# Kernel optimization log

Measured on AMD Instinct MI355X. Metric: run time of the kernel, lower is better.

Reference implementation:

```python
import jax, jax.numpy as jnp
import numpy as np

MASK_SUB = 1000000.0  # the module subtracts 1e6 from masked scores (not -inf)

def setup_inputs() -> dict:
    key = jax.random.key(0)
    kq, kk, kv = jax.random.split(key, 3)
    B, S, D = 16, 2048, 64
    q = jax.random.normal(kq, (B, S, D), dtype=jnp.float32)
    k = jax.random.normal(kk, (B, S, D), dtype=jnp.float32)
    v = jax.random.normal(kv, (B, S, D), dtype=jnp.float32)
    return {"q": q, "k": k, "v": v}

def reference(q, k, v):
    d_k = k.shape[-1]
    s = k.shape[-2]
    # scores: [b, s_q, s_k]
    scores = jnp.einsum('bqd,bkd->bqk', q, k) / jnp.sqrt(jnp.asarray(d_k, q.dtype))
    # causal mask: strictly-upper-triangular entries get 1e6 subtracted (matches torch.triu diagonal=1)
    causal = jnp.triu(jnp.ones((s, s), dtype=bool), k=1)
    scores = jnp.where(causal[None, :, :], scores - MASK_SUB, scores)
    weights = jax.nn.softmax(scores, axis=-1)
    return jnp.einsum('bqk,bkd->bqd', weights, v)
```

## Files before the change

kernel.cpp:

```cpp
#include <hip/hip_runtime.h>
#include <stdint.h>


typedef __bf16 bf16x8 __attribute__((ext_vector_type(8)));
typedef float f32x4 __attribute__((ext_vector_type(4)));

#define NB 16
#define SL 2048
#define DH 64

__device__ __forceinline__ __bf16 f2bf(float f) {
    uint32_t u = __builtin_bit_cast(uint32_t, f);
    u += 0x7FFFu + ((u >> 16) & 1u);
    uint16_t h = (uint16_t)(u >> 16);
    return __builtin_bit_cast(__bf16, h);
}

__device__ __forceinline__ void load_lds16(const void* g, void* l) {
    __builtin_amdgcn_global_load_lds(
        (const __attribute__((address_space(1))) uint32_t*)g,
        (__attribute__((address_space(3))) uint32_t*)l, 16, 0, 0);
}

__global__ __launch_bounds__(256) void prepass(
        const float* __restrict__ K, const float* __restrict__ V,
        __bf16* __restrict__ Kb, __bf16* __restrict__ Vt) {
    __shared__ float tl[64][68];
    const int b    = blockIdx.x >> 5;
    const int tile = blockIdx.x & 31;
    const int s0   = tile << 6;
    const int t    = threadIdx.x;
    const int r    = t >> 2;
    const int c0   = (t & 3) * 16;

    const float* Kp = K + ((size_t)(b * SL + s0) + r) * DH + c0;
    float4 f0 = ((const float4*)Kp)[0], f1 = ((const float4*)Kp)[1];
    float4 f2 = ((const float4*)Kp)[2], f3 = ((const float4*)Kp)[3];
    bf16x8 w0, w1;
    w0[0]=f2bf(f0.x); w0[1]=f2bf(f0.y); w0[2]=f2bf(f0.z); w0[3]=f2bf(f0.w);
    w0[4]=f2bf(f1.x); w0[5]=f2bf(f1.y); w0[6]=f2bf(f1.z); w0[7]=f2bf(f1.w);
    w1[0]=f2bf(f2.x); w1[1]=f2bf(f2.y); w1[2]=f2bf(f2.z); w1[3]=f2bf(f2.w);
    w1[4]=f2bf(f3.x); w1[5]=f2bf(f3.y); w1[6]=f2bf(f3.z); w1[7]=f2bf(f3.w);
    __bf16* Kbp = Kb + ((size_t)(b * SL + s0) + r) * DH;
    const int j0 = c0 >> 3;
    *(bf16x8*)(Kbp + ((j0       ^ (r & 7)) * 8)) = w0;
    *(bf16x8*)(Kbp + (((j0 + 1) ^ (r & 7)) * 8)) = w1;

    const float* Vp = V + ((size_t)(b * SL + s0) + r) * DH + c0;
    ((float4*)&tl[r][c0])[0] = ((const float4*)Vp)[0];
    ((float4*)&tl[r][c0])[1] = ((const float4*)Vp)[1];
    ((float4*)&tl[r][c0])[2] = ((const float4*)Vp)[2];
    ((float4*)&tl[r][c0])[3] = ((const float4*)Vp)[3];
    __syncthreads();

    __bf16* img = Vt + ((size_t)(b * 32 + tile)) * 4096;
#pragma unroll
    for (int half = 0; half < 2; ++half) {
        const int c = half * 256 + t;
        const int d = c >> 3, slot = c & 7;
        const int jj = slot ^ (d & 7);
        bf16x8 w;
#pragma unroll
        for (int e = 0; e < 8; ++e) w[e] = f2bf(tl[jj * 8 + e][d]);
        *(bf16x8*)(img + c * 8) = w;
    }
}

__global__ __launch_bounds__(256, 2) void attn_fwd(
        const float* __restrict__ Q, const __bf16* __restrict__ Kb,
        const __bf16* __restrict__ Vt, float* __restrict__ part,
        float* __restrict__ lpart) {
    __shared__ __align__(16) __bf16 lK[3][4096];
    __shared__ __align__(16) __bf16 lV[3][4096];
    __shared__ __align__(16) __bf16 lP[4][2048];

    const int bid = blockIdx.x;
    const int b   = bid & 15;
    const int j   = 39 - (bid >> 4);
    int qb, c;
    if (j < 4)        { qb = j;                 c = 0; }
    else if (j < 12)  { qb = 4 + ((j - 4) >> 1);  c = (j - 4) & 1; }
    else if (j < 24)  { int k = j - 12; qb = 8 + k / 3;    c = k % 3; }
    else              { int k = j - 24; qb = 12 + (k >> 2); c = k & 3; }
    const int nt  = 2 * qb + 2;
    const int kt0 = c * 8;
    const int kt1 = min(kt0 + 8, nt);

    const int tid  = threadIdx.x;
    const int wave = tid >> 6, lane = tid & 63, quad = lane >> 4, l16 = lane & 15;
    const int xk   = l16 & 7;
    const int qg0  = qb * 128 + wave * 16 + l16;
    const int qg1  = qg0 + 64;

    const float QSC = 0.125f * 1.44269504088896340736f;
    bf16x8 qf[2][2];
#pragma unroll
    for (int st = 0; st < 2; ++st) {
        const float* qp = Q + ((size_t)b * SL + (st ? qg1 : qg0)) * DH;
#pragma unroll
        for (int s = 0; s < 2; ++s) {
            float4 a0 = ((const float4*)(qp + s * 32 + quad * 8))[0];
            float4 a1 = ((const float4*)(qp + s * 32 + quad * 8))[1];
            qf[st][s][0] = f2bf(a0.x * QSC); qf[st][s][1] = f2bf(a0.y * QSC);
            qf[st][s][2] = f2bf(a0.z * QSC); qf[st][s][3] = f2bf(a0.w * QSC);
            qf[st][s][4] = f2bf(a1.x * QSC); qf[st][s][5] = f2bf(a1.y * QSC);
            qf[st][s][6] = f2bf(a1.z * QSC); qf[st][s][7] = f2bf(a1.w * QSC);
        }
    }

    f32x4 acc0[4], acc1[4];
#pragma unroll
    for (int t = 0; t < 4; ++t) { acc0[t] = (f32x4)0.0f; acc1[t] = (f32x4)0.0f; }
    float ls0 = 0.0f, ls1 = 0.0f;

    const __bf16* Kbase = Kb + (size_t)b * SL * DH;
    const __bf16* Vbase = Vt + (size_t)b * 32 * 4096;
    __bf16* lPw = lP[wave];

    auto stage = [&](int kt2) {
        const int bufi = kt2 % 3;
        const __bf16* Ks = Kbase + (size_t)kt2 * 4096;
        const __bf16* Vs = Vbase + (size_t)kt2 * 4096;
#pragma unroll
        for (int i2 = 0; i2 < 2; ++i2) {
            load_lds16(Ks + (size_t)(i2 * 256 + tid) * 8,
                       &lK[bufi][(i2 * 256 + wave * 64) * 8]);
            load_lds16(Vs + (size_t)(i2 * 256 + tid) * 8,
                       &lV[bufi][(i2 * 256 + wave * 64) * 8]);
        }
    };

    auto softmax_store = [&](f32x4* sc, int soff, float& ls) {
#pragma unroll
        for (int t = 0; t < 4; ++t) {
            float p0 = __builtin_amdgcn_exp2f(sc[t][0]);
            float p1 = __builtin_amdgcn_exp2f(sc[t][1]);
            float p2 = __builtin_amdgcn_exp2f(sc[t][2]);
            float p3 = __builtin_amdgcn_exp2f(sc[t][3]);
            ls += (p0 + p1) + (p2 + p3);
            uint32_t u0 = __builtin_amdgcn_perm(__builtin_bit_cast(uint32_t, p1),
                                               __builtin_bit_cast(uint32_t, p0), 0x07060302u);
            uint32_t u1 = __builtin_amdgcn_perm(__builtin_bit_cast(uint32_t, p3),
                                               __builtin_bit_cast(uint32_t, p2), 0x07060302u);
            const int cw = 2 * t + (quad >> 1);
            uint2 val; val.x = u0; val.y = u1;
            *(uint2*)&lPw[soff + l16 * 64 + ((cw ^ xk) << 3) + ((quad & 1) << 2)] = val;
        }
    };

    __builtin_amdgcn_sched_barrier(0);
    stage(kt0);
    __builtin_amdgcn_sched_barrier(0);
    stage(kt0 + 1);

    for (int kt = kt0; kt < kt1; ++kt) {
        if (kt + 1 < kt1) asm volatile("s_waitcnt vmcnt(4)" ::: "memory");
        else              asm volatile("s_waitcnt vmcnt(0)" ::: "memory");
        __builtin_amdgcn_s_barrier();
        __builtin_amdgcn_sched_barrier(0);
        if (kt + 2 < kt1) stage(kt + 2);

        const __bf16* K_ = lK[kt % 3];
        const __bf16* V_ = lV[kt % 3];

        f32x4 sc0[4], sc1[4];
#pragma unroll
        for (int t = 0; t < 4; ++t) { sc0[t] = (f32x4)0.0f; sc1[t] = (f32x4)0.0f; }
        __builtin_amdgcn_s_setprio(1);
#pragma unroll
        for (int s = 0; s < 2; ++s) {
#pragma unroll
            for (int t = 0; t < 4; ++t) {
                bf16x8 kf = *(const bf16x8*)&K_[(t * 16 + l16) * 64 + (((s * 4 + quad) ^ xk) << 3)];
                sc0[t] = __builtin_amdgcn_mfma_f32_16x16x32_bf16(kf, qf[0][s], sc0[t], 0, 0, 0);
                sc1[t] = __builtin_amdgcn_mfma_f32_16x16x32_bf16(kf, qf[1][s], sc1[t], 0, 0, 0);
            }
        }
        __builtin_amdgcn_s_setprio(0);

        if (kt >= 2 * qb) {
            const int kb = kt * 64;
#pragma unroll
            for (int t = 0; t < 4; ++t)
#pragma unroll
                for (int r = 0; r < 4; ++r) {
                    const int key = kb + t * 16 + quad * 4 + r;
                    if (key > qg0) sc0[t][r] = -1.0e30f;
                    if (key > qg1) sc1[t][r] = -1.0e30f;
                }
        }

        const bool s0live = (kt != nt - 1);
        if (s0live) softmax_store(sc0, 0, ls0);
        softmax_store(sc1, 1024, ls1);
        asm volatile("" ::: "memory");

        bf16x8 pf10 = *(const bf16x8*)&lPw[1024 + l16 * 64 + (((0 + quad) ^ xk) << 3)];
        bf16x8 pf11 = *(const bf16x8*)&lPw[1024 + l16 * 64 + (((4 + quad) ^ xk) << 3)];

        __builtin_amdgcn_s_setprio(1);
        if (s0live) {
            bf16x8 pf00 = *(const bf16x8*)&lPw[l16 * 64 + (((0 + quad) ^ xk) << 3)];
            bf16x8 pf01 = *(const bf16x8*)&lPw[l16 * 64 + (((4 + quad) ^ xk) << 3)];
#pragma unroll
            for (int t = 0; t < 4; ++t) {
                bf16x8 vf = *(const bf16x8*)&V_[(t * 16 + l16) * 64 + (((0 + quad) ^ xk) << 3)];
                acc0[t] = __builtin_amdgcn_mfma_f32_16x16x32_bf16(vf, pf00, acc0[t], 0, 0, 0);
                acc1[t] = __builtin_amdgcn_mfma_f32_16x16x32_bf16(vf, pf10, acc1[t], 0, 0, 0);
            }
#pragma unroll
            for (int t = 0; t < 4; ++t) {
                bf16x8 vf = *(const bf16x8*)&V_[(t * 16 + l16) * 64 + (((4 + quad) ^ xk) << 3)];
                acc0[t] = __builtin_amdgcn_mfma_f32_16x16x32_bf16(vf, pf01, acc0[t], 0, 0, 0);
                acc1[t] = __builtin_amdgcn_mfma_f32_16x16x32_bf16(vf, pf11, acc1[t], 0, 0, 0);
            }
        } else {
#pragma unroll
            for (int t = 0; t < 4; ++t) {
                bf16x8 vf = *(const bf16x8*)&V_[(t * 16 + l16) * 64 + (((0 + quad) ^ xk) << 3)];
                acc1[t] = __builtin_amdgcn_mfma_f32_16x16x32_bf16(vf, pf10, acc1[t], 0, 0, 0);
            }
#pragma unroll
            for (int t = 0; t < 4; ++t) {
                bf16x8 vf = *(const bf16x8*)&V_[(t * 16 + l16) * 64 + (((4 + quad) ^ xk) << 3)];
                acc1[t] = __builtin_amdgcn_mfma_f32_16x16x32_bf16(vf, pf11, acc1[t], 0, 0, 0);
            }
        }
        __builtin_amdgcn_s_setprio(0);
    }

    ls0 += __shfl_xor(ls0, 16); ls0 += __shfl_xor(ls0, 32);
    ls1 += __shfl_xor(ls1, 16); ls1 += __shfl_xor(ls1, 32);

    float* pp0 = part + ((size_t)(b * SL + qg0) * 4 + c) * DH + quad * 4;
    float* pp1 = part + ((size_t)(b * SL + qg1) * 4 + c) * DH + quad * 4;
#pragma unroll
    for (int t = 0; t < 4; ++t) {
        float4 o4;
        o4.x = acc0[t][0]; o4.y = acc0[t][1]; o4.z = acc0[t][2]; o4.w = acc0[t][3];
        *(float4*)(pp0 + t * 16) = o4;
        o4.x = acc1[t][0]; o4.y = acc1[t][1]; o4.z = acc1[t][2]; o4.w = acc1[t][3];
        *(float4*)(pp1 + t * 16) = o4;
    }
    if (quad == 0) {
        lpart[(size_t)(b * SL + qg0) * 4 + c] = ls0;
        lpart[(size_t)(b * SL + qg1) * 4 + c] = ls1;
    }
}

__global__ __launch_bounds__(256) void combine(
        const float* __restrict__ part, const float* __restrict__ lpart,
        float* __restrict__ O) {
    const int tid = threadIdx.x;
    const int r   = blockIdx.x * 16 + (tid >> 4);
    const int d4  = tid & 15;
    const int qb  = (r >> 7) & 15;
    const int nch = (2 * qb + 9) >> 3;
    float4 s = make_float4(0.f, 0.f, 0.f, 0.f);
    float ls = 0.f;
    for (int c = 0; c < nch; ++c) {
        float4 p = *(const float4*)(part + ((size_t)r * 4 + c) * DH + d4 * 4);
        s.x += p.x; s.y += p.y; s.z += p.z; s.w += p.w;
        ls += lpart[(size_t)r * 4 + c];
    }
    const float inv = 1.0f / ls;
    float4 o; o.x = s.x * inv; o.y = s.y * inv; o.z = s.z * inv; o.w = s.w * inv;
    *(float4*)(O + (size_t)r * DH + d4 * 4) = o;
}

extern "C" void kernel_launch(void* const* d_in, const int* in_sizes, int n_in,
                              void* d_out, int out_size, void* d_ws, size_t ws_size,
                              hipStream_t stream) {
    const float* q = (const float*)d_in[0];
    const float* k = (const float*)d_in[1];
    const float* v = (const float*)d_in[2];
    float* o = (float*)d_out;
    __bf16* Kb   = (__bf16*)d_ws;
    __bf16* Vt   = Kb + (size_t)NB * SL * DH;
    float*  pt   = (float*)((char*)d_ws + (8u << 20));
    float*  lp   = pt + (size_t)NB * SL * 4 * DH;
    hipLaunchKernelGGL(prepass, dim3(NB * 32), dim3(256), 0, stream, k, v, Kb, Vt);
    hipLaunchKernelGGL(attn_fwd, dim3(640), dim3(256), 0, stream, q, Kb, Vt, pt, lp);
    hipLaunchKernelGGL(combine, dim3(NB * SL / 16), dim3(256), 0, stream, pt, lp, o);
}
```

Baseline: 106.2 us.

## Read K and V tiles directly from global memory instead of LDS staging

Removes the triple-buffered LDS staging of K and V tiles (global_load_lds plus waitcnt/barrier pipeline). Each wave now reads its K and V fragments straight from global memory through the cache. Occupancy is raised to 3 blocks per SM now that LDS use is smaller. This drops the barriers and LDS traffic, but exposes global-load latency and duplicate loads across waves, with no explicit prefetch.

```diff
diff --git a/kernel.cpp b/kernel.cpp
--- a/kernel.cpp
+++ b/kernel.cpp
@@ -14,12 +14,6 @@
     u += 0x7FFFu + ((u >> 16) & 1u);
     uint16_t h = (uint16_t)(u >> 16);
     return __builtin_bit_cast(__bf16, h);
-}
-
-__device__ __forceinline__ void load_lds16(const void* g, void* l) {
-    __builtin_amdgcn_global_load_lds(
-        (const __attribute__((address_space(1))) uint32_t*)g,
-        (__attribute__((address_space(3))) uint32_t*)l, 16, 0, 0);
 }
 
 __global__ __launch_bounds__(256) void prepass(
@@ -66,12 +60,10 @@
     }
 }
 
-__global__ __launch_bounds__(256, 2) void attn_fwd(
+__global__ __launch_bounds__(256, 3) void attn_fwd(
         const float* __restrict__ Q, const __bf16* __restrict__ Kb,
         const __bf16* __restrict__ Vt, float* __restrict__ part,
         float* __restrict__ lpart) {
-    __shared__ __align__(16) __bf16 lK[3][4096];
-    __shared__ __align__(16) __bf16 lV[3][4096];
     __shared__ __align__(16) __bf16 lP[4][2048];
 
     const int bid = blockIdx.x;
@@ -116,19 +108,6 @@
     const __bf16* Kbase = Kb + (size_t)b * SL * DH;
     const __bf16* Vbase = Vt + (size_t)b * 32 * 4096;
     __bf16* lPw = lP[wave];
-
-    auto stage = [&](int kt2) {
-        const int bufi = kt2 % 3;
-        const __bf16* Ks = Kbase + (size_t)kt2 * 4096;
-        const __bf16* Vs = Vbase + (size_t)kt2 * 4096;
-#pragma unroll
-        for (int i2 = 0; i2 < 2; ++i2) {
-            load_lds16(Ks + (size_t)(i2 * 256 + tid) * 8,
-                       &lK[bufi][(i2 * 256 + wave * 64) * 8]);
-            load_lds16(Vs + (size_t)(i2 * 256 + tid) * 8,
-                       &lV[bufi][(i2 * 256 + wave * 64) * 8]);
-        }
-    };
 
     auto softmax_store = [&](f32x4* sc, int soff, float& ls) {
 #pragma unroll
@@ -148,20 +127,9 @@
         }
     };
 
-    __builtin_amdgcn_sched_barrier(0);
-    stage(kt0);
-    __builtin_amdgcn_sched_barrier(0);
-    stage(kt0 + 1);
-
     for (int kt = kt0; kt < kt1; ++kt) {
-        if (kt + 1 < kt1) asm volatile("s_waitcnt vmcnt(4)" ::: "memory");
-        else              asm volatile("s_waitcnt vmcnt(0)" ::: "memory");
-        __builtin_amdgcn_s_barrier();
-        __builtin_amdgcn_sched_barrier(0);
-        if (kt + 2 < kt1) stage(kt + 2);
-
-        const __bf16* K_ = lK[kt % 3];
-        const __bf16* V_ = lV[kt % 3];
+        const __bf16* K_ = Kbase + (size_t)kt * 4096;
+        const __bf16* V_ = Vbase + (size_t)kt * 4096;
 
         f32x4 sc0[4], sc1[4];
 #pragma unroll
```

After: 103.8 us. -2.2%, faster.
